# Performance work log

Measured on AMD Instinct MI355X. Metric: run time of the kernel, lower is better.

## Reference

```python
import jax, jax.numpy as jnp
import numpy as np

FILTER_ORDER = 49   # M
FRAME_PERIOD = 80   # P
IGNORE_GAIN = False


def linear_interpolation(b, P):
    """Upsample frame-level coeffs (..., N, D) -> (..., N*P, D).

    Matches diffsptk LinearInterpolation: replicate-pad last frame, then
    linear interpolation with align_corners=True, i.e.
    h[n*P + p] = (1 - p/P) * b[n] + (p/P) * b[min(n+1, N-1)].
    """
    if P == 1:
        return b
    N, D = b.shape[-2], b.shape[-1]
    left = b                                             # (..., N, D)
    right = jnp.concatenate([b[..., 1:, :], b[..., -1:, :]], axis=-2)  # (..., N, D)
    w = (jnp.arange(P, dtype=b.dtype) / P)[:, None]      # (P, 1)
    h = left[..., :, None, :] * (1 - w) + right[..., :, None, :] * w  # (..., N, P, D)
    return h.reshape(*b.shape[:-2], N * P, D)


def setup_inputs() -> dict:
    key = jax.random.key(0)
    k1, k2 = jax.random.split(key)
    B = 8
    N = 3000                       # number of frames
    T = N * FRAME_PERIOD           # 240000 samples
    x = jax.random.normal(k1, (B, T), dtype=jnp.float32)
    b = jax.random.normal(k2, (B, N, FILTER_ORDER + 1), dtype=jnp.float32)
    return {"x": x, "b": b}


def reference(x, b):
    M = b.shape[-1] - 1
    T = x.shape[-1]
    # per-sample filter taps, flipped so h[..., k] multiplies x[t - M + k]
    h = linear_interpolation(jnp.flip(b, axis=-1), FRAME_PERIOD)  # (B, T, M+1)
    if IGNORE_GAIN:
        h = h / h[..., -1:]
    xp = jnp.pad(x, ((0, 0), (M, 0)))                    # (B, T+M)
    idx = jnp.arange(T)[:, None] + jnp.arange(M + 1)[None, :]  # (T, M+1)
    windows = xp[:, idx]                                 # (B, T, M+1)
    y = jnp.sum(windows * h, axis=-1)                    # (B, T)
    return y
```

## Files before the change

kernel.cpp:

```cpp
#include <hip/hip_runtime.h>

constexpr int M      = 49;
constexpr int TAPS   = 50;
constexpr int P      = 80;
constexpr int BLOCK  = 256;
constexpr int NFR    = 6;
constexpr int FSTRIDE = 52;

__global__ __launch_bounds__(BLOCK) void azdf_kernel(
    const float* __restrict__ x, const float* __restrict__ b,
    float* __restrict__ y, int T, int N) {
  __shared__ float xs[BLOCK + M + 3];
  __shared__ float bs[NFR * FSTRIDE];

  const int batch = blockIdx.y;
  const int t0 = blockIdx.x * BLOCK;
  const int tid = threadIdx.x;
  const float* xb = x + (size_t)batch * T;
  const float* bb = b + (size_t)batch * N * TAPS;

  for (int i = tid; i < BLOCK + M; i += BLOCK) {
    int xi = t0 - M + i;
    xs[i] = (xi >= 0 && xi < T) ? xb[xi] : 0.0f;
  }

  const int n_first = t0 / P;
  for (int i = tid; i < NFR * TAPS; i += BLOCK) {
    int f = i / TAPS;
    int k = i - f * TAPS;
    int n = n_first + f;
    if (n > N - 1) n = N - 1;
    bs[f * FSTRIDE + k] = bb[(size_t)n * TAPS + k];
  }
  __syncthreads();

  const int t = t0 + tid;
  if (t < T) {
    const int n = t / P;
    const float w = (float)(t - n * P) * (1.0f / (float)P);
    const float* c0 = &bs[(n - n_first) * FSTRIDE];
    const float* c1 = c0 + FSTRIDE;
    float s0 = 0.0f, s1 = 0.0f;
#pragma unroll
    for (int k = 0; k < TAPS; ++k) {
      float xv = xs[tid + M - k];
      s0 = fmaf(xv, c0[k], s0);
      s1 = fmaf(xv, c1[k], s1);
    }
    y[(size_t)batch * T + t] = (1.0f - w) * s0 + w * s1;
  }
}

extern "C" void kernel_launch(void* const* d_in, const int* in_sizes, int n_in,
                              void* d_out, int out_size, void* d_ws, size_t ws_size,
                              hipStream_t stream) {
  const float* x = (const float*)d_in[0];
  const float* b = (const float*)d_in[1];
  float* y = (float*)d_out;

  const int B = 8;
  const int N = in_sizes[1] / (B * TAPS);
  const int T = N * P;

  dim3 grid((T + BLOCK - 1) / BLOCK, B);
  azdf_kernel<<<grid, BLOCK, 0, stream>>>(x, b, y, T, N);
}
```

Measured before the change: 78.60 us.

## Register-block 8 outputs per thread with x window cached in registers

Each thread now computes 8 consecutive outputs. It keeps a 60-element sliding window of x in registers and reads the filter taps as float4 from shared memory, so each tap load is reused across 8 outputs. Tiles grow to 2048 samples per block, with 28 frames of coefficients staged. Outputs are written as float4 stores. This cuts LDS traffic per FMA. In exchange, register pressure rises and fewer blocks are launched, which may reduce occupancy.

```diff
diff --git a/kernel.cpp b/kernel.cpp
--- a/kernel.cpp
+++ b/kernel.cpp
@@ -4,25 +4,28 @@
 constexpr int TAPS   = 50;
 constexpr int P      = 80;
 constexpr int BLOCK  = 256;
-constexpr int NFR    = 6;
+constexpr int R      = 8;
+constexpr int TILE   = BLOCK * R;
+constexpr int NFR    = 28;
 constexpr int FSTRIDE = 52;
 
 __global__ __launch_bounds__(BLOCK) void azdf_kernel(
     const float* __restrict__ x, const float* __restrict__ b,
     float* __restrict__ y, int T, int N) {
-  __shared__ float xs[BLOCK + M + 3];
+  __shared__ float xs[TILE + M + 15];
   __shared__ float bs[NFR * FSTRIDE];
 
   const int batch = blockIdx.y;
-  const int t0 = blockIdx.x * BLOCK;
+  const int t0 = blockIdx.x * TILE;
   const int tid = threadIdx.x;
   const float* xb = x + (size_t)batch * T;
   const float* bb = b + (size_t)batch * N * TAPS;
 
-  for (int i = tid; i < BLOCK + M; i += BLOCK) {
+  for (int i = tid; i < TILE + M; i += BLOCK) {
     int xi = t0 - M + i;
     xs[i] = (xi >= 0 && xi < T) ? xb[xi] : 0.0f;
   }
+  if (tid < 15) xs[TILE + M + tid] = 0.0f;
 
   const int n_first = t0 / P;
   for (int i = tid; i < NFR * TAPS; i += BLOCK) {
@@ -34,20 +37,73 @@
   }
   __syncthreads();
 
-  const int t = t0 + tid;
-  if (t < T) {
-    const int n = t / P;
-    const float w = (float)(t - n * P) * (1.0f / (float)P);
-    const float* c0 = &bs[(n - n_first) * FSTRIDE];
-    const float* c1 = c0 + FSTRIDE;
-    float s0 = 0.0f, s1 = 0.0f;
+  const int t_base = t0 + tid * R;
+  if (t_base >= T) return;
+
+  float xr[60];
 #pragma unroll
-    for (int k = 0; k < TAPS; ++k) {
-      float xv = xs[tid + M - k];
-      s0 = fmaf(xv, c0[k], s0);
-      s1 = fmaf(xv, c1[k], s1);
+  for (int j = 0; j < 15; ++j) {
+    float4 v = *(const float4*)&xs[tid * R + 4 * j];
+    xr[4 * j + 0] = v.x; xr[4 * j + 1] = v.y;
+    xr[4 * j + 2] = v.z; xr[4 * j + 3] = v.w;
+  }
+
+  const int n = t_base / P;
+  const float* c0 = &bs[(n - n_first) * FSTRIDE];
+  const float* c1 = c0 + FSTRIDE;
+
+  float s0[R], s1[R];
+#pragma unroll
+  for (int r = 0; r < R; ++r) { s0[r] = 0.0f; s1[r] = 0.0f; }
+
+#pragma unroll
+  for (int kc = 0; kc < 48; kc += 4) {
+    float4 a0 = *(const float4*)&c0[kc];
+    float4 a1 = *(const float4*)&c1[kc];
+    const float av0[4] = {a0.x, a0.y, a0.z, a0.w};
+    const float av1[4] = {a1.x, a1.y, a1.z, a1.w};
+#pragma unroll
+    for (int kk = 0; kk < 4; ++kk) {
+      const int k = kc + kk;
+#pragma unroll
+      for (int r = 0; r < R; ++r) {
+        float xv = xr[M + r - k];
+        s0[r] = fmaf(xv, av0[kk], s0[r]);
+        s1[r] = fmaf(xv, av1[kk], s1[r]);
+      }
     }
-    y[(size_t)batch * T + t] = (1.0f - w) * s0 + w * s1;
+  }
+  {
+    float2 a0 = *(const float2*)&c0[48];
+    float2 a1 = *(const float2*)&c1[48];
+#pragma unroll
+    for (int r = 0; r < R; ++r) {
+      float xv = xr[M + r - 48];
+      s0[r] = fmaf(xv, a0.x, s0[r]);
+      s1[r] = fmaf(xv, a1.x, s1[r]);
+    }
+#pragma unroll
+    for (int r = 0; r < R; ++r) {
+      float xv = xr[M + r - 49];
+      s0[r] = fmaf(xv, a0.y, s0[r]);
+      s1[r] = fmaf(xv, a1.y, s1[r]);
+    }
+  }
+
+  const int phase = t_base - n * P;
+  float out[R];
+#pragma unroll
+  for (int r = 0; r < R; ++r) {
+    float w = (float)(phase + r) * (1.0f / (float)P);
+    out[r] = (1.0f - w) * s0[r] + w * s1[r];
+  }
+
+  float* yp = y + (size_t)batch * T + t_base;
+  if (t_base + R <= T) {
+    *(float4*)(yp + 0) = make_float4(out[0], out[1], out[2], out[3]);
+    *(float4*)(yp + 4) = make_float4(out[4], out[5], out[6], out[7]);
+  } else {
+    for (int r = 0; r < R && t_base + r < T; ++r) yp[r] = out[r];
   }
 }
 
@@ -62,6 +118,6 @@
   const int N = in_sizes[1] / (B * TAPS);
   const int T = N * P;
 
-  dim3 grid((T + BLOCK - 1) / BLOCK, B);
+  dim3 grid((T + TILE - 1) / TILE, B);
   azdf_kernel<<<grid, BLOCK, 0, stream>>>(x, b, y, T, N);
 }
```

New measurement: 75.44 us. -4.0%, faster.
